# Kernel tuning notes

Hardware: AMD Instinct MI355X
Metric: run time of the kernel (lower is better)

## Reference

```python
import jax, jax.numpy as jnp
import numpy as np

K = 512   # per-head dim == input dim
H = 8     # heads

def setup_inputs() -> dict:
    key = jax.random.key(0)
    ks = jax.random.split(key, 6)
    b, t = 4, 2048
    x = jax.random.normal(ks[0], (b, t, K), dtype=jnp.float32)
    s = 0.02
    Wq = jax.random.normal(ks[1], (K, K * H), dtype=jnp.float32) * s
    Wk = jax.random.normal(ks[2], (K, K * H), dtype=jnp.float32) * s
    Wv = jax.random.normal(ks[3], (K, K * H), dtype=jnp.float32) * s
    Wo = jax.random.normal(ks[4], (K * H, K), dtype=jnp.float32) * s
    bo = jnp.zeros((K,), dtype=jnp.float32)
    return {"x": x, "Wq": Wq, "Wk": Wk, "Wv": Wv, "Wo": Wo, "bo": bo}

def reference(x, Wq, Wk, Wv, Wo, bo):
    b, t, _ = x.shape
    scale = K ** 0.25
    # rearrange 'b t (k h) -> (b h) t k' == reshape (b,t,K,H) then move h next to b
    def split_heads(y):
        return y.reshape(b, t, K, H).transpose(0, 3, 1, 2)  # [b,h,t,K]
    q = split_heads(x @ Wq) / scale
    k_ = split_heads(x @ Wk) / scale
    v = split_heads(x @ Wv)
    dot = jnp.einsum('bhtk,bhsk->bhts', q, k_)      # [b,h,t,t]
    attn = jax.nn.softmax(dot, axis=-1)
    o = jnp.einsum('bhts,bhsk->bhtk', attn, v)      # [b,h,t,K]
    # '(b h) t k -> b t (h k)': heads outer in concat
    o = o.transpose(0, 2, 1, 3).reshape(b, t, H * K)
    return o @ Wo + bo
```

## Files before the change

kernel.cpp:

```cpp
#include <hip/hip_runtime.h>

typedef unsigned short u16;
typedef unsigned char u8;
typedef unsigned int u32;
typedef long i64;
typedef __attribute__((ext_vector_type(8))) short bf16x8;
typedef __attribute__((ext_vector_type(4))) float f32x4;
typedef __attribute__((ext_vector_type(4))) u16 u16x4;

__device__ __forceinline__ u16 f2bf(float f) {
  u32 u = __builtin_bit_cast(u32, f);
  return (u16)((u + 0x7FFFu + ((u >> 16) & 1u)) >> 16);
}
__device__ __forceinline__ u8 f2fp8(float f) {
  int w = __builtin_amdgcn_cvt_pk_fp8_f32(f, 0.f, 0, false);
  return (u8)(w & 0xff);
}

__device__ __forceinline__ f32x4 mfma16(bf16x8 a, bf16x8 b, f32x4 c) {
  return __builtin_amdgcn_mfma_f32_16x16x32_bf16(a, b, c, 0, 0, 0);
}
__device__ __forceinline__ f32x4 mfma16f8(i64 a, i64 b, f32x4 c) {
  return __builtin_amdgcn_mfma_f32_16x16x32_fp8_fp8(a, b, c, 0, 0, 0);
}

__device__ __forceinline__ void gload16(const void* g, void* l) {
  __builtin_amdgcn_global_load_lds(
      (const __attribute__((address_space(1))) unsigned int*)g,
      (__attribute__((address_space(3))) unsigned int*)l, 16, 0, 0);
}

__device__ __forceinline__ u32 cvtpk(float lo, float hi) {
  u32 r;
  asm volatile("v_cvt_pk_bf16_f32 %0, %1, %2" : "=v"(r) : "v"(lo), "v"(hi));
  return r;
}


__global__ void pack_x_kernel(const float* __restrict__ x, u16* __restrict__ xb) {
  const int i = blockIdx.x * 256 + threadIdx.x;
  const float4 v = ((const float4*)x)[i];
  u16x4 o;
  o[0] = f2bf(v.x); o[1] = f2bf(v.y); o[2] = f2bf(v.z); o[3] = f2bf(v.w);
  ((u16x4*)xb)[i] = o;
}

__global__ void pack_wqkv_t(const float* __restrict__ W, u16* __restrict__ Wp) {
  __shared__ u16 tile[64][72];
  const int t = threadIdx.x;
  const int c0 = blockIdx.x * 64, dd0 = blockIdx.y * 64;
#pragma unroll
  for (int s = 0; s < 4; ++s) {
    const int r = s * 16 + (t >> 4);
    const int q = (t & 15) * 4;
    const float4 v = *(const float4*)&W[(size_t)(dd0 + r) * 4096 + c0 + q];
    tile[r][q + 0] = f2bf(v.x); tile[r][q + 1] = f2bf(v.y);
    tile[r][q + 2] = f2bf(v.z); tile[r][q + 3] = f2bf(v.w);
  }
  __syncthreads();
#pragma unroll
  for (int s = 0; s < 4; ++s) {
    const int cl = s * 16 + (t >> 4);
    const int u = t & 15;
    const int cg = c0 + cl;
    const int orow = (cg & 7) * 512 + (cg >> 3);
    u16x4 o;
#pragma unroll
    for (int i = 0; i < 4; ++i) o[i] = tile[u * 4 + i][cl];
    *(u16x4*)&Wp[(size_t)orow * 512 + dd0 + u * 4] = o;
  }
}

__global__ void pack_wo_t(const float* __restrict__ W, u16* __restrict__ Wp) {
  __shared__ u16 tile[64][72];
  const int t = threadIdx.x;
  const int k0 = blockIdx.x * 64, n0 = blockIdx.y * 64;
#pragma unroll
  for (int s = 0; s < 4; ++s) {
    const int r = s * 16 + (t >> 4);
    const int q = (t & 15) * 4;
    const float4 v = *(const float4*)&W[(size_t)(k0 + r) * 512 + n0 + q];
    tile[r][q + 0] = f2bf(v.x); tile[r][q + 1] = f2bf(v.y);
    tile[r][q + 2] = f2bf(v.z); tile[r][q + 3] = f2bf(v.w);
  }
  __syncthreads();
#pragma unroll
  for (int s = 0; s < 4; ++s) {
    const int cl = s * 16 + (t >> 4);
    const int u = t & 15;
    u16x4 o;
#pragma unroll
    for (int i = 0; i < 4; ++i) o[i] = tile[u * 4 + i][cl];
    *(u16x4*)&Wp[(size_t)(n0 + cl) * 4096 + k0 + u * 4] = o;
  }
}


template <int MODE, int BN>
__global__ __launch_bounds__(256, 2) void gemm_bf16(
    const u16* __restrict__ A, const u16* __restrict__ B,
    void* __restrict__ Cout, const float* __restrict__ bias,
    int Kd, float scale) {
  constexpr int JT = BN / 32;
  __shared__ u16 Al[128 * 64];
  __shared__ u16 Bl[BN * 64];
  const int tid = threadIdx.x;
  const int lane = tid & 63;
  const int w = tid >> 6, wm = w >> 1, wn = w & 1;
  const int l15 = lane & 15, lg = lane >> 4;
  const int m0 = blockIdx.y * 128, n0 = blockIdx.x * BN;

  f32x4 acc[4][JT];
#pragma unroll
  for (int i = 0; i < 4; ++i)
#pragma unroll
    for (int j = 0; j < JT; ++j) acc[i][j] = {};

  const int nk = Kd >> 6;
  for (int kt = 0; kt < nk; ++kt) {
    __syncthreads();
    const int k0 = kt << 6;
#pragma unroll
    for (int s = 0; s < 4; ++s) {
      const int chunk = s * 256 + tid;
      const int row = chunk >> 3, c = chunk & 7;
      const int cs = c ^ (row & 7);
      gload16(A + (size_t)(m0 + row) * Kd + k0 + cs * 8, &Al[chunk * 8]);
    }
#pragma unroll
    for (int s = 0; s < BN / 32; ++s) {
      const int chunk = s * 256 + tid;
      const int row = chunk >> 3, c = chunk & 7;
      const int cs = c ^ (row & 7);
      gload16(B + (size_t)(n0 + row) * Kd + k0 + cs * 8, &Bl[chunk * 8]);
    }
    __syncthreads();
#pragma unroll
    for (int kk = 0; kk < 2; ++kk) {
      bf16x8 af[4], bfr[JT];
      const int ch = kk * 4 + lg;
#pragma unroll
      for (int i = 0; i < 4; ++i) {
        const int ar = wm * 64 + i * 16 + l15;
        af[i] = *(const bf16x8*)&Al[ar * 64 + ((ch ^ (ar & 7)) * 8)];
      }
#pragma unroll
      for (int j = 0; j < JT; ++j) {
        const int br = wn * (BN / 2) + j * 16 + l15;
        bfr[j] = *(const bf16x8*)&Bl[br * 64 + ((ch ^ (br & 7)) * 8)];
      }
#pragma unroll
      for (int i = 0; i < 4; ++i)
#pragma unroll
        for (int j = 0; j < JT; ++j)
          acc[i][j] = mfma16(af[i], bfr[j], acc[i][j]);
    }
  }

#pragma unroll
  for (int i = 0; i < 4; ++i) {
    const int gr0 = m0 + wm * 64 + i * 16 + lg * 4;
#pragma unroll
    for (int j = 0; j < JT; ++j) {
      const int gc = n0 + wn * (BN / 2) + j * 16 + l15;
      if constexpr (MODE == 0) {
        u8* O = (u8*)Cout;
        const int h = gc >> 9, d = gc & 511;
#pragma unroll
        for (int r = 0; r < 4; ++r) {
          const int grr = gr0 + r;
          const int bb = grr >> 11, t = grr & 2047;
          O[((size_t)((bb * 8 + h) * 2048 + t) << 9) + d] = f2fp8(acc[i][j][r] * scale);
        }
      } else if constexpr (MODE == 1) {
        u16* O = (u16*)Cout;
        const int h = gc >> 9, d = gc & 511;
        const int bb = gr0 >> 11, t = gr0 & 2047;
        u16x4 pk;
#pragma unroll
        for (int r = 0; r < 4; ++r) pk[r] = f2bf(acc[i][j][r]);
        *(u16x4*)&O[((size_t)((bb * 8 + h) * 512 + d) << 11) + t] = pk;
      } else {
        float* O = (float*)Cout;
        const float bv = bias[gc];
#pragma unroll
        for (int r = 0; r < 4; ++r)
          O[(size_t)(gr0 + r) * 512 + gc] = acc[i][j][r] + bv;
      }
    }
  }
}


__global__ __launch_bounds__(512, 2) void attn_kernel(
    const u8* __restrict__ Qg, const u8* __restrict__ Kg,
    const u16* __restrict__ Vtg, u16* __restrict__ Og, int nbh_pxcd) {
  __shared__ u8 K8[2][32 * 512];
  __shared__ u16 V3[3][512 * 32];
  __shared__ u16 P_lds[2][4][2][16][32];
  __shared__ float Lsum[8][2][16];

  const int tid = threadIdx.x;
  const int lane = tid & 63;
  const int w = tid >> 6;
  const int pr = w >> 1, whalf = w & 1;
  const int l15 = lane & 15, lg = lane >> 4;

  const int bid = blockIdx.x;
  const int x8 = bid & 7, rest = bid >> 3;
  const int qt = rest & 15;
  const int bh = x8 * nbh_pxcd + (rest >> 4);

  const u8* Qb = Qg + (size_t)bh * 2048 * 512;
  const u8* Kb = Kg + (size_t)bh * 2048 * 512;
  const u16* Vb = Vtg + (size_t)bh * 2048 * 512;

  i64 qf8[2][16];
#pragma unroll
  for (int qtile = 0; qtile < 2; ++qtile) {
    const int qrow = qt * 128 + pr * 32 + qtile * 16 + l15;
    const u8* qp = Qb + (size_t)qrow * 512 + lg * 8;
#pragma unroll
    for (int cc = 0; cc < 16; ++cc) qf8[qtile][cc] = *(const i64*)(qp + cc * 32);
  }

  f32x4 acc[2][16];
#pragma unroll
  for (int i = 0; i < 2; ++i)
#pragma unroll
    for (int j = 0; j < 16; ++j) acc[i][j] = {};
  float lsum0 = 0.f, lsum1 = 0.f;

  const int krow = whalf * 16 + l15;
  const int kswz = (krow & 15) << 1;

#define STAGE_K8(tile, buf)                                                   \
  {                                                                           \
    _Pragma("unroll") for (int s_ = 0; s_ < 2; ++s_) {                        \
      const int ch = s_ * 512 + tid;                                          \
      const int row = ch >> 5, p_ = ch & 31;                                  \
      const int ps = p_ ^ ((row & 15) << 1);                                  \
      gload16(Kb + (size_t)((tile) * 32 + row) * 512 + ps * 16,               \
              &K8[buf][ch * 16]);                                             \
    }                                                                         \
  }
#define STAGE_V(tile, buf)                                                    \
  {                                                                           \
    _Pragma("unroll") for (int s_ = 0; s_ < 4; ++s_) {                        \
      const int chunk = s_ * 512 + tid;                                       \
      const int row = chunk >> 2, c_ = chunk & 3;                             \
      const int cs = c_ ^ ((row >> 1) & 3);                                   \
      gload16(Vb + (size_t)row * 2048 + (tile) * 32 + cs * 8,                 \
              &V3[buf][chunk * 8]);                                           \
    }                                                                         \
  }

#define PV_LAG(par, vbuf)                                                     \
  {                                                                           \
    bf16x8 pfr0 = *(const bf16x8*)&P_lds[par][pr][0][l15][lg * 8];            \
    bf16x8 pfr1 = *(const bf16x8*)&P_lds[par][pr][1][l15][lg * 8];            \
    _Pragma("unroll") for (int dtile = 0; dtile < 16; ++dtile) {              \
      const int drow = whalf * 256 + dtile * 16 + l15;                        \
      const int pos = lg ^ ((drow >> 1) & 3);                                 \
      bf16x8 vf = *(const bf16x8*)&V3[vbuf][drow * 32 + pos * 8];             \
      acc[0][dtile] = mfma16(vf, pfr0, acc[0][dtile]);                        \
      acc[1][dtile] = mfma16(vf, pfr1, acc[1][dtile]);                        \
    }                                                                         \
  }

  STAGE_K8(0, 0);
  STAGE_V(0, 0);
  asm volatile("s_waitcnt vmcnt(0)" ::: "memory");
  __builtin_amdgcn_s_barrier();

  int vstage = 1;
  int vread = 2;

  for (int t = 0; t < 64; ++t) {
    const int cur = t & 1;

    if (t < 63) {
      STAGE_K8(t + 1, cur ^ 1);
      STAGE_V(t + 1, vstage);
    }

    f32x4 s0a = {}, s0b = {}, s1a = {}, s1b = {};
    {
      const u8* kbase = &K8[cur][krow * 512 + (lg & 1) * 8];
      const int phalf = lg >> 1;
#pragma unroll
      for (int cc = 0; cc < 8; ++cc) {
        const int p = (cc * 2 + phalf) ^ kswz;
        i64 kf = *(const i64*)(kbase + p * 16);
        s0a = mfma16f8(kf, qf8[0][cc], s0a);
        s1a = mfma16f8(kf, qf8[1][cc], s1a);
      }
#pragma unroll
      for (int cc = 8; cc < 16; ++cc) {
        const int p = (cc * 2 + phalf) ^ kswz;
        i64 kf = *(const i64*)(kbase + p * 16);
        s0b = mfma16f8(kf, qf8[0][cc], s0b);
        s1b = mfma16f8(kf, qf8[1][cc], s1b);
      }
    }
    f32x4 s0, s1;
#pragma unroll
    for (int r = 0; r < 4; ++r) {
      s0[r] = __expf(s0a[r] + s0b[r]);
      lsum0 += s0[r];
      s1[r] = __expf(s1a[r] + s1b[r]);
      lsum1 += s1[r];
    }

    {
      const int kvbase = whalf * 16 + lg * 4;
      u32 a0 = cvtpk(s0[0], s0[1]), a1 = cvtpk(s0[2], s0[3]);
      u32 b0 = cvtpk(s1[0], s1[1]), b1 = cvtpk(s1[2], s1[3]);
      u16x4 pk0 = __builtin_bit_cast(u16x4, ((unsigned long long)a1 << 32) | a0);
      u16x4 pk1 = __builtin_bit_cast(u16x4, ((unsigned long long)b1 << 32) | b0);
      *(u16x4*)&P_lds[cur][pr][0][l15][kvbase] = pk0;
      *(u16x4*)&P_lds[cur][pr][1][l15][kvbase] = pk1;
    }

    if (t > 0) PV_LAG(cur ^ 1, vread);

    asm volatile("s_waitcnt vmcnt(0) lgkmcnt(0)" ::: "memory");
    __builtin_amdgcn_s_barrier();

    vstage = (vstage == 2) ? 0 : vstage + 1;
    vread = (vread == 2) ? 0 : vread + 1;
  }

  PV_LAG(1, vread);

  lsum0 += __shfl_xor(lsum0, 16, 64);
  lsum0 += __shfl_xor(lsum0, 32, 64);
  lsum1 += __shfl_xor(lsum1, 16, 64);
  lsum1 += __shfl_xor(lsum1, 32, 64);
  if (lane < 16) {
    Lsum[w][0][l15] = lsum0;
    Lsum[w][1][l15] = lsum1;
  }
  __syncthreads();
  const float inv0 = 1.0f / (Lsum[w][0][l15] + Lsum[w ^ 1][0][l15]);
  const float inv1 = 1.0f / (Lsum[w][1][l15] + Lsum[w ^ 1][1][l15]);

  const int bb = bh >> 3, h = bh & 7;
#pragma unroll
  for (int qtile = 0; qtile < 2; ++qtile) {
    const float inv = qtile ? inv1 : inv0;
    const int q = qt * 128 + pr * 32 + qtile * 16 + l15;
    u16* orow_p = Og + (size_t)(bb * 2048 + q) * 4096 + h * 512 + whalf * 256;
#pragma unroll
    for (int dtile = 0; dtile < 16; ++dtile) {
      u16x4 pk;
#pragma unroll
      for (int r = 0; r < 4; ++r) pk[r] = f2bf(acc[qtile][dtile][r] * inv);
      *(u16x4*)(orow_p + dtile * 16 + lg * 4) = pk;
    }
  }
#undef STAGE_K8
#undef STAGE_V
#undef PV_LAG
}


extern "C" void kernel_launch(void* const* d_in, const int* in_sizes, int n_in,
                              void* d_out, int out_size, void* d_ws, size_t ws_size,
                              hipStream_t stream) {
  const float* x = (const float*)d_in[0];
  const float* Wq = (const float*)d_in[1];
  const float* Wk = (const float*)d_in[2];
  const float* Wv = (const float*)d_in[3];
  const float* Wo = (const float*)d_in[4];
  const float* bo = (const float*)d_in[5];
  float* out = (float*)d_out;

  const size_t MB = 1ull << 20;
  int BB;
  if (ws_size >= 216 * MB) BB = 4;
  else if (ws_size >= 120 * MB) BB = 2;
  else BB = 1;

  char* ws = (char*)d_ws;
  u16* xb  = (u16*)(ws);
  u16* Wqp = (u16*)(ws + 8 * MB);
  u16* Wkp = (u16*)(ws + 12 * MB);
  u16* Wvp = (u16*)(ws + 16 * MB);
  u16* Wot = (u16*)(ws + 20 * MB);
  u8*  Qg  = (u8*)(ws + 24 * MB);
  u8*  Kg  = (u8*)(ws + (24 + 8 * (size_t)BB) * MB);
  u16* Vtg = (u16*)(ws + (24 + 16 * (size_t)BB) * MB);
  u16* Og  = (u16*)(ws + (24 + 32 * (size_t)BB) * MB);

  pack_x_kernel<<<dim3(4096), dim3(256), 0, stream>>>(x, xb);
  pack_wqkv_t<<<dim3(64, 8), dim3(256), 0, stream>>>(Wq, Wqp);
  pack_wqkv_t<<<dim3(64, 8), dim3(256), 0, stream>>>(Wk, Wkp);
  pack_wqkv_t<<<dim3(64, 8), dim3(256), 0, stream>>>(Wv, Wvp);
  pack_wo_t<<<dim3(64, 8), dim3(256), 0, stream>>>(Wo, Wot);

  const float qk_scale = 0.21022410381342865f;

  const int nchunk = 4 / BB;
  for (int c = 0; c < nchunk; ++c) {
    const u16* Ax = xb + (size_t)c * BB * 2048 * 512;
    gemm_bf16<0, 128><<<dim3(32, BB * 16), dim3(256), 0, stream>>>(Ax, Wqp, (void*)Qg, nullptr, 512, qk_scale);
    gemm_bf16<0, 128><<<dim3(32, BB * 16), dim3(256), 0, stream>>>(Ax, Wkp, (void*)Kg, nullptr, 512, qk_scale);
    gemm_bf16<1, 128><<<dim3(32, BB * 16), dim3(256), 0, stream>>>(Ax, Wvp, (void*)Vtg, nullptr, 512, 1.0f);

    attn_kernel<<<dim3(16 * BB * 8), dim3(512), 0, stream>>>(Qg, Kg, Vtg, Og, BB);

    gemm_bf16<2, 64><<<dim3(8, BB * 16), dim3(256), 0, stream>>>(
        Og, Wot, (void*)(out + (size_t)c * BB * 2048 * 512), bo, 4096, 1.0f);
  }
}
```

Before: 524.0 us.

## Load K fragments directly from pre-tiled global layout into registers, shrink attention blocks

```diff
diff --git a/kernel.cpp b/kernel.cpp
--- a/kernel.cpp
+++ b/kernel.cpp
@@ -180,6 +180,16 @@
 #pragma unroll
         for (int r = 0; r < 4; ++r) pk[r] = f2bf(acc[i][j][r]);
         *(u16x4*)&O[((size_t)((bb * 8 + h) * 512 + d) << 11) + t] = pk;
+      } else if constexpr (MODE == 3) {
+        u8* O = (u8*)Cout;
+        const int h = gc >> 9, k = gc & 511;
+#pragma unroll
+        for (int r = 0; r < 4; ++r) {
+          const int grr = gr0 + r;
+          const int bb = grr >> 11, t = grr & 2047;
+          O[((((size_t)(bb * 8 + h) * 64 + (t >> 5)) * 32 + (k >> 4)) * 32 + (t & 31)) * 16 +
+            (k & 15)] = f2fp8(acc[i][j][r] * scale);
+        }
       } else {
         float* O = (float*)Cout;
         const float bv = bias[gc];
@@ -192,13 +202,12 @@
 }
 
 
-__global__ __launch_bounds__(512, 2) void attn_kernel(
-    const u8* __restrict__ Qg, const u8* __restrict__ Kg,
+__global__ __launch_bounds__(256, 2) void attn_kernel(
+    const u8* __restrict__ Qg, const u8* __restrict__ K4g,
     const u16* __restrict__ Vtg, u16* __restrict__ Og, int nbh_pxcd) {
-  __shared__ u8 K8[2][32 * 512];
-  __shared__ u16 V3[3][512 * 32];
-  __shared__ u16 P_lds[2][4][2][16][32];
-  __shared__ float Lsum[8][2][16];
+  __shared__ u16 Vt_lds[2][512 * 32];
+  __shared__ u16 P_lds[2][2][16][32];
+  __shared__ float Lsum[4][2][16];
 
   const int tid = threadIdx.x;
   const int lane = tid & 63;
@@ -208,21 +217,23 @@
 
   const int bid = blockIdx.x;
   const int x8 = bid & 7, rest = bid >> 3;
-  const int qt = rest & 15;
-  const int bh = x8 * nbh_pxcd + (rest >> 4);
+  const int qt = rest & 31;
+  const int bh = x8 * nbh_pxcd + (rest >> 5);
 
   const u8* Qb = Qg + (size_t)bh * 2048 * 512;
-  const u8* Kb = Kg + (size_t)bh * 2048 * 512;
+  const u8* K4b = K4g + (size_t)bh * 2048 * 512;
   const u16* Vb = Vtg + (size_t)bh * 2048 * 512;
 
   i64 qf8[2][16];
 #pragma unroll
   for (int qtile = 0; qtile < 2; ++qtile) {
-    const int qrow = qt * 128 + pr * 32 + qtile * 16 + l15;
+    const int qrow = qt * 64 + pr * 32 + qtile * 16 + l15;
     const u8* qp = Qb + (size_t)qrow * 512 + lg * 8;
 #pragma unroll
     for (int cc = 0; cc < 16; ++cc) qf8[qtile][cc] = *(const i64*)(qp + cc * 32);
   }
+
+  const int klane = (lg >> 1) * 512 + (whalf * 16 + l15) * 16 + (lg & 1) * 8;
 
   f32x4 acc[2][16];
 #pragma unroll
@@ -231,78 +242,50 @@
     for (int j = 0; j < 16; ++j) acc[i][j] = {};
   float lsum0 = 0.f, lsum1 = 0.f;
 
-  const int krow = whalf * 16 + l15;
-  const int kswz = (krow & 15) << 1;
-
-#define STAGE_K8(tile, buf)                                                   \
-  {                                                                           \
-    _Pragma("unroll") for (int s_ = 0; s_ < 2; ++s_) {                        \
-      const int ch = s_ * 512 + tid;                                          \
-      const int row = ch >> 5, p_ = ch & 31;                                  \
-      const int ps = p_ ^ ((row & 15) << 1);                                  \
-      gload16(Kb + (size_t)((tile) * 32 + row) * 512 + ps * 16,               \
-              &K8[buf][ch * 16]);                                             \
-    }                                                                         \
-  }
 #define STAGE_V(tile, buf)                                                    \
   {                                                                           \
-    _Pragma("unroll") for (int s_ = 0; s_ < 4; ++s_) {                        \
-      const int chunk = s_ * 512 + tid;                                       \
+    _Pragma("unroll") for (int s_ = 0; s_ < 8; ++s_) {                        \
+      const int chunk = s_ * 256 + tid;                                       \
       const int row = chunk >> 2, c_ = chunk & 3;                             \
       const int cs = c_ ^ ((row >> 1) & 3);                                   \
       gload16(Vb + (size_t)row * 2048 + (tile) * 32 + cs * 8,                 \
-              &V3[buf][chunk * 8]);                                           \
+              &Vt_lds[buf][chunk * 8]);                                       \
     }                                                                         \
   }
 
-#define PV_LAG(par, vbuf)                                                     \
-  {                                                                           \
-    bf16x8 pfr0 = *(const bf16x8*)&P_lds[par][pr][0][l15][lg * 8];            \
-    bf16x8 pfr1 = *(const bf16x8*)&P_lds[par][pr][1][l15][lg * 8];            \
-    _Pragma("unroll") for (int dtile = 0; dtile < 16; ++dtile) {              \
-      const int drow = whalf * 256 + dtile * 16 + l15;                        \
-      const int pos = lg ^ ((drow >> 1) & 3);                                 \
-      bf16x8 vf = *(const bf16x8*)&V3[vbuf][drow * 32 + pos * 8];             \
-      acc[0][dtile] = mfma16(vf, pfr0, acc[0][dtile]);                        \
-      acc[1][dtile] = mfma16(vf, pfr1, acc[1][dtile]);                        \
-    }                                                                         \
-  }
-
-  STAGE_K8(0, 0);
   STAGE_V(0, 0);
+  i64 kf[16];
+  {
+    const u8* kp = K4b + klane;
+#pragma unroll
+    for (int cc = 0; cc < 16; ++cc) kf[cc] = *(const i64*)(kp + cc * 1024);
+  }
   asm volatile("s_waitcnt vmcnt(0)" ::: "memory");
   __builtin_amdgcn_s_barrier();
 
-  int vstage = 1;
-  int vread = 2;
-
   for (int t = 0; t < 64; ++t) {
     const int cur = t & 1;
 
+    if (t < 63) STAGE_V(t + 1, cur ^ 1);
+
+    f32x4 s0a = {}, s0b = {}, s1a = {}, s1b = {};
+#pragma unroll
+    for (int cc = 0; cc < 8; ++cc) {
+      s0a = mfma16f8(kf[cc], qf8[0][cc], s0a);
+      s1a = mfma16f8(kf[cc], qf8[1][cc], s1a);
+    }
+#pragma unroll
+    for (int cc = 8; cc < 16; ++cc) {
+      s0b = mfma16f8(kf[cc], qf8[0][cc], s0b);
+      s1b = mfma16f8(kf[cc], qf8[1][cc], s1b);
+    }
+
     if (t < 63) {
-      STAGE_K8(t + 1, cur ^ 1);
-      STAGE_V(t + 1, vstage);
-    }
-
-    f32x4 s0a = {}, s0b = {}, s1a = {}, s1b = {};
-    {
-      const u8* kbase = &K8[cur][krow * 512 + (lg & 1) * 8];
-      const int phalf = lg >> 1;
-#pragma unroll
-      for (int cc = 0; cc < 8; ++cc) {
-        const int p = (cc * 2 + phalf) ^ kswz;
-        i64 kf = *(const i64*)(kbase + p * 16);
-        s0a = mfma16f8(kf, qf8[0][cc], s0a);
-        s1a = mfma16f8(kf, qf8[1][cc], s1a);
-      }
-#pragma unroll
-      for (int cc = 8; cc < 16; ++cc) {
-        const int p = (cc * 2 + phalf) ^ kswz;
-        i64 kf = *(const i64*)(kbase + p * 16);
-        s0b = mfma16f8(kf, qf8[0][cc], s0b);
-        s1b = mfma16f8(kf, qf8[1][cc], s1b);
-      }
-    }
+      const u8* kp = K4b + ((size_t)(t + 1) << 14) + klane;
+#pragma unroll
+      for (int cc = 0; cc < 16; ++cc) kf[cc] = *(const i64*)(kp + cc * 1024);
+    }
+
     f32x4 s0, s1;
 #pragma unroll
     for (int r = 0; r < 4; ++r) {
@@ -318,20 +301,28 @@
       u32 b0 = cvtpk(s1[0], s1[1]), b1 = cvtpk(s1[2], s1[3]);
       u16x4 pk0 = __builtin_bit_cast(u16x4, ((unsigned long long)a1 << 32) | a0);
       u16x4 pk1 = __builtin_bit_cast(u16x4, ((unsigned long long)b1 << 32) | b0);
-      *(u16x4*)&P_lds[cur][pr][0][l15][kvbase] = pk0;
-      *(u16x4*)&P_lds[cur][pr][1][l15][kvbase] = pk1;
-    }
-
-    if (t > 0) PV_LAG(cur ^ 1, vread);
+      *(u16x4*)&P_lds[pr][0][l15][kvbase] = pk0;
+      *(u16x4*)&P_lds[pr][1][l15][kvbase] = pk1;
+    }
+    asm volatile("s_waitcnt lgkmcnt(0)" ::: "memory");
+    __builtin_amdgcn_s_barrier();
+
+    {
+      bf16x8 pfr0 = *(const bf16x8*)&P_lds[pr][0][l15][lg * 8];
+      bf16x8 pfr1 = *(const bf16x8*)&P_lds[pr][1][l15][lg * 8];
+#pragma unroll
+      for (int dtile = 0; dtile < 16; ++dtile) {
+        const int drow = whalf * 256 + dtile * 16 + l15;
+        const int pos = lg ^ ((drow >> 1) & 3);
+        bf16x8 vf = *(const bf16x8*)&Vt_lds[cur][drow * 32 + pos * 8];
+        acc[0][dtile] = mfma16(vf, pfr0, acc[0][dtile]);
+        acc[1][dtile] = mfma16(vf, pfr1, acc[1][dtile]);
+      }
+    }
 
     asm volatile("s_waitcnt vmcnt(0) lgkmcnt(0)" ::: "memory");
     __builtin_amdgcn_s_barrier();
-
-    vstage = (vstage == 2) ? 0 : vstage + 1;
-    vread = (vread == 2) ? 0 : vread + 1;
-  }
-
-  PV_LAG(1, vread);
+  }
 
   lsum0 += __shfl_xor(lsum0, 16, 64);
   lsum0 += __shfl_xor(lsum0, 32, 64);
@@ -349,7 +340,7 @@
 #pragma unroll
   for (int qtile = 0; qtile < 2; ++qtile) {
     const float inv = qtile ? inv1 : inv0;
-    const int q = qt * 128 + pr * 32 + qtile * 16 + l15;
+    const int q = qt * 64 + pr * 32 + qtile * 16 + l15;
     u16* orow_p = Og + (size_t)(bb * 2048 + q) * 4096 + h * 512 + whalf * 256;
 #pragma unroll
     for (int dtile = 0; dtile < 16; ++dtile) {
@@ -359,9 +350,7 @@
       *(u16x4*)(orow_p + dtile * 16 + lg * 4) = pk;
     }
   }
-#undef STAGE_K8
 #undef STAGE_V
-#undef PV_LAG
 }
 
 
@@ -405,10 +394,10 @@
   for (int c = 0; c < nchunk; ++c) {
     const u16* Ax = xb + (size_t)c * BB * 2048 * 512;
     gemm_bf16<0, 128><<<dim3(32, BB * 16), dim3(256), 0, stream>>>(Ax, Wqp, (void*)Qg, nullptr, 512, qk_scale);
-    gemm_bf16<0, 128><<<dim3(32, BB * 16), dim3(256), 0, stream>>>(Ax, Wkp, (void*)Kg, nullptr, 512, qk_scale);
+    gemm_bf16<3, 128><<<dim3(32, BB * 16), dim3(256), 0, stream>>>(Ax, Wkp, (void*)Kg, nullptr, 512, qk_scale);
     gemm_bf16<1, 128><<<dim3(32, BB * 16), dim3(256), 0, stream>>>(Ax, Wvp, (void*)Vtg, nullptr, 512, 1.0f);
 
-    attn_kernel<<<dim3(16 * BB * 8), dim3(512), 0, stream>>>(Qg, Kg, Vtg, Og, BB);
+    attn_kernel<<<dim3(32 * BB * 8), dim3(256), 0, stream>>>(Qg, Kg, Vtg, Og, BB);
 
     gemm_bf16<2, 64><<<dim3(8, BB * 16), dim3(256), 0, stream>>>(
         Og, Wot, (void*)(out + (size_t)c * BB * 2048 * 512), bo, 4096, 1.0f);
```

After: 708.1 us. 35.1% more time.
